# Optimization experiments

Hardware: AMD Instinct MI355X
Metric: run time of the kernel (lower is better)

The kernel has to match this reference:

```python
import jax, jax.numpy as jnp
import numpy as np
from jax.scipy.special import logsumexp

NEG = -1e8
B, M, R, D, H = 32, 24, 384, 2048, 16

def setup_inputs() -> dict:
    key = jax.random.key(0)
    ks = jax.random.split(key, 12)
    inp = {
        'region': jax.random.normal(ks[0], (B, R, D), dtype=jnp.float32),
        'aff': jax.random.normal(ks[1], (B, M, R, 1), dtype=jnp.float32),
        'aff_gt': jax.random.uniform(ks[2], (B, M, R, 1), dtype=jnp.float32),
        'n_mentions': jax.random.randint(ks[3], (B,), 8, M + 1, dtype=jnp.int32),
        'n_regions': jax.random.randint(ks[4], (B,), R // 2, R + 1, dtype=jnp.int32),
        # learned params: tran0/tran1: Linear(d_region,16); tran: Linear(16,1)
        't0_w': jax.random.normal(ks[5], (H, D), dtype=jnp.float32) / np.sqrt(D),
        't0_b': jnp.zeros((H,), dtype=jnp.float32),
        't1_w': jax.random.normal(ks[6], (H, D), dtype=jnp.float32) / np.sqrt(D),
        't1_b': jnp.zeros((H,), dtype=jnp.float32),
        'tr_w': jax.random.normal(ks[7], (1, H), dtype=jnp.float32) / np.sqrt(H),
        'tr_b': jnp.zeros((1,), dtype=jnp.float32),
    }
    return inp


def reference(region, aff, aff_gt, n_mentions, n_regions, t0_w, t0_b, t1_w, t1_b, tr_w, tr_b):
    # masks for padded regions / mentions
    reg_mask = jnp.arange(R)[None, :] < n_regions[:, None]        # (B,R)
    men_mask = jnp.arange(M)[None, :] < n_mentions[:, None]       # (B,M)

    # soft-label normalization (_aff_acti / _aff_norm / _aff_norm_log in torch)
    a = jnp.where(aff_gt[..., 0] >= 0.5, aff_gt[..., 0], 0.0)     # (B,M,R)
    a = a * reg_mask[:, None, :] * men_mask[:, :, None]
    s = a.sum(-1, keepdims=True)
    reward = a / jnp.where(s > 0, s, 1.0)                          # (B,M,R)
    reward_log = jnp.where(reward > 0, jnp.log(jnp.where(reward > 0, reward, 1.0)), NEG)
    active = (s[..., 0] > 0) & men_mask                            # (B,M) mentions with >=1 gold region

    # transition matrix (tran_context='none'): tran[b,i,j] = tran(relu(tran0(r_i)+tran1(r_j)))
    h0 = region @ t0_w.T + t0_b                                    # (B,R,H)
    h1 = region @ t1_w.T + t1_b                                    # (B,R,H)
    h = jax.nn.relu(h0[:, :, None, :] + h1[:, None, :, :])         # (B,R,R,H)
    tran = jnp.einsum('brsh,h->brs', h, tr_w[0]) + tr_b[0]         # (B,R,R): [i=to, j=from]

    emit = aff[..., 0]                                             # (B,M,R)
    alpha0 = jnp.where(reg_mask, 0.0, NEG)                         # padded tags excluded from logsumexp
    score0 = jnp.zeros((B, R), dtype=region.dtype)
    rprev0 = jnp.zeros((B, R), dtype=region.dtype)
    hasp0 = jnp.zeros((B,), dtype=bool)

    def step(carry, xs):
        alpha, score, rprev, hasp = carry
        e, rw, rl, act = xs                                        # (B,R)x3, (B,)
        alpha_t = logsumexp(alpha[:, None, :] + tran, axis=2)      # (B,R)
        score_t = jnp.sum((score[:, None, :] + tran) * rprev[:, None, :], axis=2)
        do_t = (act & hasp)[:, None]
        alpha = jnp.where(do_t, alpha_t, alpha)
        score = jnp.where(do_t, score_t, score)
        am = act[:, None]
        alpha = jnp.where(am, alpha + e, alpha)
        score = jnp.where(am, score + e - rl, score)
        rprev = jnp.where(am, rw, rprev)
        hasp = hasp | act
        return (alpha, score, rprev, hasp), None

    xs = (jnp.moveaxis(emit, 1, 0), jnp.moveaxis(reward, 1, 0),
          jnp.moveaxis(reward_log, 1, 0), active.T)
    (alpha, score, rprev, hasp), _ = jax.lax.scan(step, (alpha0, score0, rprev0, hasp0), xs)

    fwd = logsumexp(alpha, axis=1)                                 # (B,)
    gold = jnp.sum(score * rprev, axis=1)                          # (B,)
    fwd = jnp.where(hasp, fwd, 0.0)
    gold = jnp.where(hasp, gold, 0.0)
    denom = jnp.maximum(n_mentions.sum(), 1).astype(region.dtype)
    return jnp.sum(fwd - gold) / denom
```

## Files before the change

kernel.cpp:

```cpp
#include <hip/hip_runtime.h>

#define NEGV (-100000000.0f)
typedef __attribute__((ext_vector_type(2))) float f32x2;
typedef __attribute__((ext_vector_type(8))) short bf16x8;
typedef __attribute__((ext_vector_type(4))) float f32x4v;

constexpr int BB = 32, MM = 24, RR = 384, DD = 2048;
constexpr int EPITCH = 400;

static __device__ __forceinline__ unsigned pk2bf(float a, float b) {
  unsigned au = __float_as_uint(a) + 0x8000u;
  unsigned bu = __float_as_uint(b) + 0x8000u;
  return (au >> 16) | (bu & 0xffff0000u);
}

__global__ __launch_bounds__(256) void kA(const float* __restrict__ region,
    const float* __restrict__ t0w, const float* __restrict__ t0b,
    const float* __restrict__ t1w, const float* __restrict__ t1b,
    float* __restrict__ h0h1) {
  __shared__ unsigned short Abuf[2][32 * 128];
  __shared__ unsigned short Bbuf[2][32 * 128];
  const int tid = threadIdx.x;
  const int row0 = blockIdx.x * 32;

  const int srow = tid >> 3;
  const int sq = tid & 7;
  const float* aSrc = region + (size_t)(row0 + srow) * DD + sq * 16;
  const float* bSrc = ((srow < 16) ? (t0w + (size_t)srow * DD)
                                   : (t1w + (size_t)(srow - 16) * DD)) + sq * 16;

  auto LOADS = [&](float4* s, int t) {
    const int d0 = t * 128;
#pragma unroll
    for (int i = 0; i < 4; ++i) s[i] = *(const float4*)(aSrc + d0 + i * 4);
#pragma unroll
    for (int i = 0; i < 4; ++i) s[4 + i] = *(const float4*)(bSrc + d0 + i * 4);
  };
  const int wbase = srow * 256 + sq * 32;
  const int wxor = (srow & 7) << 4;
  auto WRITES = [&](const float4* s, int buf) {
    unsigned char* Ab = (unsigned char*)&Abuf[buf][0];
    unsigned char* Bb = (unsigned char*)&Bbuf[buf][0];
#pragma unroll
    for (int i = 0; i < 2; ++i) {
      float4 x = s[i * 2], y = s[i * 2 + 1];
      uint4 pk;
      pk.x = pk2bf(x.x, x.y); pk.y = pk2bf(x.z, x.w);
      pk.z = pk2bf(y.x, y.y); pk.w = pk2bf(y.z, y.w);
      *(uint4*)(Ab + ((wbase + i * 16) ^ wxor)) = pk;
      float4 u = s[4 + i * 2], v = s[4 + i * 2 + 1];
      uint4 qk;
      qk.x = pk2bf(u.x, u.y); qk.y = pk2bf(u.z, u.w);
      qk.z = pk2bf(v.x, v.y); qk.w = pk2bf(v.z, v.w);
      *(uint4*)(Bb + ((wbase + i * 16) ^ wxor)) = qk;
    }
  };

  const int w = tid >> 6;
  const int rt = w & 1;
  const int ht = w >> 1;
  const int lane = tid & 63;
  const int arow = rt * 16 + (lane & 15);
  const int bh = lane & 15;
  const int brow = ht * 16 + bh;
  const int koff = (lane >> 4) * 8;
  const int axor = (arow & 7) << 4;
  const int bxor = (brow & 7) << 4;

  f32x4v acc = {0.f, 0.f, 0.f, 0.f};
  auto MFMAT = [&](int buf) {
    const unsigned char* Ab = (const unsigned char*)&Abuf[buf][0];
    const unsigned char* Bb = (const unsigned char*)&Bbuf[buf][0];
#pragma unroll
    for (int kk = 0; kk < 4; ++kk) {
      const int kb = (kk * 32 + koff) * 2;
      bf16x8 av = *(const bf16x8*)(Ab + ((arow * 256 + kb) ^ axor));
      bf16x8 bv = *(const bf16x8*)(Bb + ((brow * 256 + kb) ^ bxor));
      acc = __builtin_amdgcn_mfma_f32_16x16x32_bf16(av, bv, acc, 0, 0, 0);
    }
  };

  float4 sA[8], sB[8], sC[8];
  LOADS(sA, 0);
  WRITES(sA, 0);
  LOADS(sB, 1);
  LOADS(sC, 2);
  for (int t = 0; t < 16; t += 3) {
    __syncthreads();
    if (t + 1 < 16) WRITES(sB, (t + 1) & 1);
    if (t + 3 < 16) LOADS(sA, t + 3);
    MFMAT(t & 1);
    if (t + 1 < 16) {
      __syncthreads();
      if (t + 2 < 16) WRITES(sC, (t + 2) & 1);
      if (t + 4 < 16) LOADS(sB, t + 4);
      MFMAT((t + 1) & 1);
    }
    if (t + 2 < 16) {
      __syncthreads();
      if (t + 3 < 16) WRITES(sA, (t + 3) & 1);
      if (t + 5 < 16) LOADS(sC, t + 5);
      MFMAT(t & 1);
    }
  }

  const float bias = (ht == 0) ? t0b[bh] : t1b[bh];
#pragma unroll
  for (int i = 0; i < 4; ++i) {
    const int rg = row0 + rt * 16 + (lane >> 4) * 4 + i;
    h0h1[(size_t)rg * 32 + ht * 16 + bh] = acc[i] + bias;
  }
}

__global__ __launch_bounds__(384) void kYT(const float* __restrict__ h0h1,
    const float* __restrict__ trw, const float* __restrict__ trb,
    const float* __restrict__ gt, const float* __restrict__ aff,
    const int* __restrict__ nmen, const int* __restrict__ nreg,
    int* __restrict__ mlist, int* __restrict__ kcnt, float* __restrict__ Em,
    float* __restrict__ bilinP, unsigned char* __restrict__ expb,
    float* __restrict__ expTmax) {
  __shared__ float h1T[16][388];
  __shared__ float h0L[48][16];
  __shared__ float Tl[48][388];
  __shared__ float RP[MM][392];
  __shared__ float part[48][26];
  __shared__ float rsumL[MM], EmL[MM];
  __shared__ int mlistL[MM];
  __shared__ int kcntL;
  const int b = blockIdx.x & 31;
  const int chunk = blockIdx.x >> 5;
  const int r0 = chunk * 48;
  const int tid = threadIdx.x;
  const int lane = tid & 63;
  const int wv = tid >> 6;
  const int nm = nmen[b], nr = nreg[b];

  for (int m = wv; m < MM; m += 6) {
    const size_t bm = (size_t)(b * MM + m);
    float p = 0.f, t1 = 0.f, t2 = 0.f;
#pragma unroll
    for (int i = 0; i < 6; ++i) {
      int s = lane * 6 + i;
      float g = gt[bm * RR + s];
      float a = (g >= 0.5f && s < nr && m < nm) ? g : 0.f;
      float e = aff[bm * RR + s];
      p += a;
      t1 += a * e;
      t2 += (a > 0.f) ? a * __logf(a) : 0.f;
    }
#pragma unroll
    for (int off = 32; off > 0; off >>= 1) {
      p += __shfl_xor(p, off);
      t1 += __shfl_xor(t1, off);
      t2 += __shfl_xor(t2, off);
    }
    if (lane == 0) {
      rsumL[m] = p;
      EmL[m] = (p > 0.f) ? (t1 - t2) / p + __logf(p) : 0.f;
    }
  }
  __syncthreads();
  if (tid == 0) {
    int c = 0;
    for (int m = 0; m < MM; ++m)
      if (rsumL[m] > 0.f) mlistL[c++] = m;
    kcntL = c;
    for (int j = c; j < MM; ++j) mlistL[j] = 0;
  }
  __syncthreads();
  if (chunk == 0 && tid < MM) {
    Em[b * MM + tid] = EmL[tid];
    mlist[b * MM + tid] = mlistL[tid];
    if (tid == 0) kcnt[b] = kcntL;
  }
  const int K = kcntL;

  for (int h = 0; h < 16; ++h)
    for (int s = tid; s < RR; s += 384)
      h1T[h][s] = h0h1[((size_t)b * RR + s) * 32 + 16 + h];
  for (int i = tid; i < 768; i += 384) {
    int row = i >> 4, h = i & 15;
    h0L[row][h] = h0h1[((size_t)b * RR + r0 + row) * 32 + h];
  }
  for (int j = 0; j < MM; ++j) {
    if (j < K) {
      int m = mlistL[j];
      float inv = 1.f / rsumL[m];
      for (int s = tid; s < RR; s += 384) {
        float g = gt[((size_t)(b * MM + m)) * RR + s];
        RP[j][s] = (g >= 0.5f && s < nr) ? g * inv : 0.f;
      }
    } else {
      for (int s = tid; s < RR; s += 384) RP[j][s] = 0.f;
    }
  }
  float w0[16];
#pragma unroll
  for (int h = 0; h < 16; ++h) w0[h] = trw[h];
  const float tb = trb[0];
  __syncthreads();

  const int r = tid >> 3;
  const int jq = tid & 7;
  const int gr = r0 + r;

  for (int i = 0; i < 48; ++i) {
    const int s = jq + 8 * i;
    float a = tb;
#pragma unroll
    for (int h = 0; h < 16; ++h)
      a += fmaxf(h0L[r][h] + h1T[h][s], 0.f) * w0[h];
    Tl[r][s] = a;
  }
  __syncthreads();

  {
    float rmax = -3.0e38f;
    for (int c = 0; c < 48; c += 4) {
      float4 v = *(const float4*)&Tl[r][jq * 48 + c];
      rmax = fmaxf(rmax, fmaxf(fmaxf(v.x, v.y), fmaxf(v.z, v.w)));
    }
    rmax = fmaxf(rmax, __shfl_xor(rmax, 1));
    rmax = fmaxf(rmax, __shfl_xor(rmax, 2));
    rmax = fmaxf(rmax, __shfl_xor(rmax, 4));
    if (jq == 0) expTmax[b * RR + gr] = __expf(rmax);
    unsigned char* obase = expb + ((size_t)b * RR + gr) * RR + jq * 48;
#pragma unroll
    for (int c16 = 0; c16 < 3; ++c16) {
      int w4[4];
#pragma unroll
      for (int ii = 0; ii < 4; ++ii) {
        float4 v = *(const float4*)&Tl[r][jq * 48 + c16 * 16 + ii * 4];
        int pk = __builtin_amdgcn_cvt_pk_fp8_f32(__expf(v.x - rmax),
                                                 __expf(v.y - rmax), 0, false);
        pk = __builtin_amdgcn_cvt_pk_fp8_f32(__expf(v.z - rmax),
                                             __expf(v.w - rmax), pk, true);
        w4[ii] = pk;
      }
      *(int4*)(obase + c16 * 16) = make_int4(w4[0], w4[1], w4[2], w4[3]);
    }
  }

  float acc[3] = {0, 0, 0};
  for (int s0 = 0; s0 < RR; s0 += 4) {
    float4 tv = *(const float4*)&Tl[r][s0];
#pragma unroll
    for (int jj = 0; jj < 3; ++jj) {
      const float4 p0 = *(const float4*)&RP[jq * 3 + jj][s0];
      acc[jj] = fmaf(tv.x, p0.x, acc[jj]);
      acc[jj] = fmaf(tv.y, p0.y, acc[jj]);
      acc[jj] = fmaf(tv.z, p0.z, acc[jj]);
      acc[jj] = fmaf(tv.w, p0.w, acc[jj]);
    }
  }
#pragma unroll
  for (int jj = 0; jj < 3; ++jj) {
    const int jp = jq * 3 + jj;
    const int j = jp + 1;
    part[r][j] = (j < K) ? RP[j][gr] * acc[jj] : 0.f;
  }
  __syncthreads();
  if (tid < MM) {
    const int j = tid;
    float s = 0.f;
    if (j >= 1) {
#pragma unroll 4
      for (int rr2 = 0; rr2 < 48; ++rr2) s += part[rr2][j];
    }
    bilinP[(size_t)(b * 8 + chunk) * MM + j] = s;
  }
}

__global__ __launch_bounds__(512, 1) void kD(
    const unsigned char* __restrict__ expb, const float* __restrict__ expTmax,
    const float* __restrict__ aff, const int* __restrict__ nreg,
    const int* __restrict__ mlist, const int* __restrict__ kcnt,
    const float* __restrict__ Em, const float* __restrict__ bilinP,
    float* __restrict__ result) {
  __shared__ unsigned char eT[RR * EPITCH];
  __shared__ float tf[2][RR];
  __shared__ unsigned int tq[RR / 4];
  __shared__ float wred[2][8];
  __shared__ float fred[8];

  const int b = blockIdx.x;
  const int tid = threadIdx.x;
  const int w = tid >> 6;
  const int lane = tid & 63;
  const int r = lane & 15;
  const int q = lane >> 4;
  const bool act = (r == 0);
  const int nr = nreg[b];

  const int K = kcnt[b];
  if (K == 0) {
    if (tid == 0) result[b] = 0.f;
    return;
  }

  {
    const uint4* src = (const uint4*)(expb + (size_t)b * RR * RR);
#pragma unroll
    for (int j = 0; j < 18; ++j) {
      const int i = tid + j * 512;
      uint4 v = src[i];
      const int row = i / 24;
      const int c = (i - row * 24) * 16;
      *(uint4*)(eT + row * EPITCH + c) = v;
    }
  }
  __syncthreads();

  long long af0[12], af1[12], af2[12];
  {
    const int base = (w * 48 + r) * EPITCH + q * 8;
#pragma unroll
    for (int kt = 0; kt < 12; ++kt) {
      af0[kt] = *(const long long*)(eT + base + kt * 32);
      af1[kt] = *(const long long*)(eT + base + 16 * EPITCH + kt * 32);
      af2[kt] = *(const long long*)(eT + base + 32 * EPITCH + kt * 32);
    }
  }

  float sF4[3][4], eraw4[3][4];
  if (act) {
#pragma unroll
    for (int rt = 0; rt < 3; ++rt) {
      const int rowb = w * 48 + rt * 16 + q * 4;
      *(float4*)sF4[rt] = *(const float4*)&expTmax[b * RR + rowb];
      const int m0 = mlist[b * MM];
      *(float4*)eraw4[rt] =
          *(const float4*)(aff + ((size_t)(b * MM + m0)) * RR + rowb);
    }
  }

  float L = 0.f;

  for (int k = 0; k < K; ++k) {
    const int wpar = (k + 1) & 1;

    float nraw4[3][4] = {{0, 0, 0, 0}, {0, 0, 0, 0}, {0, 0, 0, 0}};
    if (act && k + 1 < K) {
      const int mn = mlist[b * MM + k + 1];
#pragma unroll
      for (int rt = 0; rt < 3; ++rt) {
        const int rowb = w * 48 + rt * 16 + q * 4;
        *(float4*)nraw4[rt] =
            *(const float4*)(aff + ((size_t)(b * MM + mn)) * RR + rowb);
      }
    }

    float tv[3][4] = {{0, 0, 0, 0}, {0, 0, 0, 0}, {0, 0, 0, 0}};
    if (k == 0) {
      if (act) {
#pragma unroll
        for (int rt = 0; rt < 3; ++rt)
#pragma unroll
          for (int i = 0; i < 4; ++i) {
            const int row = w * 48 + rt * 16 + q * 4 + i;
            tv[rt][i] = (row < nr) ? __expf(eraw4[rt][i]) : 0.f;
          }
      }
    } else {
      f32x4v acc0 = {0.f, 0.f, 0.f, 0.f}, acc1 = {0.f, 0.f, 0.f, 0.f},
             acc2 = {0.f, 0.f, 0.f, 0.f};
#pragma unroll
      for (int kt = 0; kt < 12; ++kt) {
        long long bf =
            *(const long long*)((const unsigned char*)tq + kt * 32 + q * 8);
        bf = act ? bf : 0ll;
        acc0 = __builtin_amdgcn_mfma_f32_16x16x32_fp8_fp8(af0[kt], bf, acc0, 0, 0, 0);
        acc1 = __builtin_amdgcn_mfma_f32_16x16x32_fp8_fp8(af1[kt], bf, acc1, 0, 0, 0);
        acc2 = __builtin_amdgcn_mfma_f32_16x16x32_fp8_fp8(af2[kt], bf, acc2, 0, 0, 0);
      }
      if (act) {
#pragma unroll
        for (int i = 0; i < 4; ++i) {
          tv[0][i] = acc0[i] * (__expf(eraw4[0][i]) * sF4[0][i] * 0.00390625f);
          tv[1][i] = acc1[i] * (__expf(eraw4[1][i]) * sF4[1][i] * 0.00390625f);
          tv[2][i] = acc2[i] * (__expf(eraw4[2][i]) * sF4[2][i] * 0.00390625f);
        }
      }
    }

    float lm = 0.f;
    if (act) {
#pragma unroll
      for (int rt = 0; rt < 3; ++rt) {
        const int rowb = w * 48 + rt * 16 + q * 4;
        *(float4*)&tf[wpar][rowb] =
            make_float4(tv[rt][0], tv[rt][1], tv[rt][2], tv[rt][3]);
        lm = fmaxf(lm, fmaxf(fmaxf(tv[rt][0], tv[rt][1]),
                             fmaxf(tv[rt][2], tv[rt][3])));
      }
#pragma unroll
      for (int rt = 0; rt < 3; ++rt)
#pragma unroll
        for (int i = 0; i < 4; ++i) eraw4[rt][i] = nraw4[rt][i];
    }
    lm = fmaxf(lm, __shfl_xor(lm, 16));
    lm = fmaxf(lm, __shfl_xor(lm, 32));
    if (lane == 0) wred[wpar][w] = lm;
    __syncthreads();

    if (k + 1 < K) {
      float4 z0 = *(const float4*)&wred[wpar][0];
      float4 z1 = *(const float4*)&wred[wpar][4];
      float zm = fmaxf(fmaxf(fmaxf(z0.x, z0.y), fmaxf(z0.z, z0.w)),
                       fmaxf(fmaxf(z1.x, z1.y), fmaxf(z1.z, z1.w)));
      L += __logf(zm);
      const float bscale = 256.f / zm;
      if (tid < 96) {
        float4 v = *(const float4*)&tf[wpar][tid * 4];
        int pk = __builtin_amdgcn_cvt_pk_fp8_f32(v.x * bscale, v.y * bscale,
                                                 0, false);
        pk = __builtin_amdgcn_cvt_pk_fp8_f32(v.z * bscale, v.w * bscale,
                                             pk, true);
        tq[tid] = (unsigned)pk;
      }
      __syncthreads();
    }
  }

  const int fpar = K & 1;
  float fp = (tid < RR) ? tf[fpar][tid] : 0.f;
#pragma unroll
  for (int off = 32; off > 0; off >>= 1) fp += __shfl_xor(fp, off);
  if (lane == 0) fred[w] = fp;
  __syncthreads();
  if (tid == 0) {
    float fs = 0.f;
#pragma unroll
    for (int i = 0; i < 8; ++i) fs += fred[i];
    const float fwd = L + __logf(fmaxf(fs, 1e-37f));
    float gold = Em[b * MM + mlist[b * MM + 0]];
    for (int j = 1; j < K; ++j) {
      float bil = 0.f;
#pragma unroll
      for (int c = 0; c < 8; ++c) bil += bilinP[(size_t)(b * 8 + c) * MM + j];
      gold += bil + Em[b * MM + mlist[b * MM + j]];
    }
    result[b] = fwd - gold;
  }
}

__global__ void kE(const float* __restrict__ result, const int* __restrict__ nmen,
                   float* __restrict__ out) {
  if (threadIdx.x == 0 && blockIdx.x == 0) {
    float s = 0.f;
    int d = 0;
    for (int b = 0; b < 32; ++b) { s += result[b]; d += nmen[b]; }
    if (d < 1) d = 1;
    out[0] = s / (float)d;
  }
}

extern "C" void kernel_launch(void* const* d_in, const int* in_sizes, int n_in,
                              void* d_out, int out_size, void* d_ws, size_t ws_size,
                              hipStream_t stream) {
  const float* region = (const float*)d_in[0];
  const float* aff    = (const float*)d_in[1];
  const float* gt     = (const float*)d_in[2];
  const int*   nmen   = (const int*)d_in[3];
  const int*   nreg   = (const int*)d_in[4];
  const float* t0w    = (const float*)d_in[5];
  const float* t0b    = (const float*)d_in[6];
  const float* t1w    = (const float*)d_in[7];
  const float* t1b    = (const float*)d_in[8];
  const float* trw    = (const float*)d_in[9];
  const float* trb    = (const float*)d_in[10];
  float* out = (float*)d_out;
  char* ws = (char*)d_ws;

  size_t off = 0;
  auto alloc = [&](size_t bytes) {
    void* p = ws + off;
    off += (bytes + 255) & ~(size_t)255;
    return p;
  };
  float*         h0h1    = (float*)alloc((size_t)BB * RR * 32 * 4);
  unsigned char* expb    = (unsigned char*)alloc((size_t)BB * RR * RR);
  float*         expTmax = (float*)alloc((size_t)BB * RR * 4);
  int*           mlist   = (int*)alloc((size_t)BB * MM * 4);
  int*           kcnt    = (int*)alloc((size_t)BB * 4);
  float*         Em      = (float*)alloc((size_t)BB * MM * 4);
  float*         bilinP  = (float*)alloc((size_t)BB * 8 * MM * 4);
  float*         result  = (float*)alloc((size_t)BB * 4);

  kA<<<(BB * RR) / 32, 256, 0, stream>>>(region, t0w, t0b, t1w, t1b, h0h1);
  kYT<<<256, 384, 0, stream>>>(h0h1, trw, trb, gt, aff, nmen, nreg,
                               mlist, kcnt, Em, bilinP, expb, expTmax);
  kD<<<BB, 512, 0, stream>>>(expb, expTmax, aff, nreg, mlist, kcnt, Em,
                             bilinP, result);
  kE<<<1, 64, 0, stream>>>(result, nmen, out);
}
```

Measured before the change: 105.5 us.

## Compute transition tile from register-held h1 and use bf16 MFMA for bilinear products

In kYT, each thread now holds its column's h1 vector in registers and reads h0 rows straight from global memory when computing the transition tile. This removes the h1T/h0L shared staging and one barrier. The Tl×RP bilinear reduction moves from scalar FMA loops to bf16 16x16x32 MFMA, with RP padded to 32 rows. Converting to bf16 lowers the precision of the gold-score term, and padding RP adds zero-fill work.

```diff
diff --git a/kernel.cpp b/kernel.cpp
--- a/kernel.cpp
+++ b/kernel.cpp
@@ -119,10 +119,8 @@
     int* __restrict__ mlist, int* __restrict__ kcnt, float* __restrict__ Em,
     float* __restrict__ bilinP, unsigned char* __restrict__ expb,
     float* __restrict__ expTmax) {
-  __shared__ float h1T[16][388];
-  __shared__ float h0L[48][16];
   __shared__ float Tl[48][388];
-  __shared__ float RP[MM][392];
+  __shared__ float RP[32][392];
   __shared__ float part[48][26];
   __shared__ float rsumL[MM], EmL[MM];
   __shared__ int mlistL[MM];
@@ -175,14 +173,7 @@
   }
   const int K = kcntL;
 
-  for (int h = 0; h < 16; ++h)
-    for (int s = tid; s < RR; s += 384)
-      h1T[h][s] = h0h1[((size_t)b * RR + s) * 32 + 16 + h];
-  for (int i = tid; i < 768; i += 384) {
-    int row = i >> 4, h = i & 15;
-    h0L[row][h] = h0h1[((size_t)b * RR + r0 + row) * 32 + h];
-  }
-  for (int j = 0; j < MM; ++j) {
+  for (int j = 0; j < 32; ++j) {
     if (j < K) {
       int m = mlistL[j];
       float inv = 1.f / rsumL[m];
@@ -194,27 +185,43 @@
       for (int s = tid; s < RR; s += 384) RP[j][s] = 0.f;
     }
   }
+
   float w0[16];
 #pragma unroll
   for (int h = 0; h < 16; ++h) w0[h] = trw[h];
   const float tb = trb[0];
+  const int s = tid;
+  float h1r[16];
+  {
+    const float* hp = h0h1 + ((size_t)b * RR + s) * 32 + 16;
+    *(float4*)&h1r[0] = *(const float4*)(hp);
+    *(float4*)&h1r[4] = *(const float4*)(hp + 4);
+    *(float4*)&h1r[8] = *(const float4*)(hp + 8);
+    *(float4*)&h1r[12] = *(const float4*)(hp + 12);
+  }
+  for (int r4 = 0; r4 < 48; r4 += 4) {
+    const float* p0 = h0h1 + ((size_t)b * RR + r0 + r4) * 32;
+    float a0 = tb, a1 = tb, a2 = tb, a3 = tb;
+#pragma unroll
+    for (int h = 0; h < 16; ++h) {
+      const float hv = h1r[h];
+      const float wvv = w0[h];
+      a0 += fmaxf(p0[h] + hv, 0.f) * wvv;
+      a1 += fmaxf(p0[32 + h] + hv, 0.f) * wvv;
+      a2 += fmaxf(p0[64 + h] + hv, 0.f) * wvv;
+      a3 += fmaxf(p0[96 + h] + hv, 0.f) * wvv;
+    }
+    Tl[r4][s] = a0;
+    Tl[r4 + 1][s] = a1;
+    Tl[r4 + 2][s] = a2;
+    Tl[r4 + 3][s] = a3;
+  }
   __syncthreads();
 
-  const int r = tid >> 3;
-  const int jq = tid & 7;
-  const int gr = r0 + r;
-
-  for (int i = 0; i < 48; ++i) {
-    const int s = jq + 8 * i;
-    float a = tb;
-#pragma unroll
-    for (int h = 0; h < 16; ++h)
-      a += fmaxf(h0L[r][h] + h1T[h][s], 0.f) * w0[h];
-    Tl[r][s] = a;
-  }
-  __syncthreads();
-
   {
+    const int r = tid >> 3;
+    const int jq = tid & 7;
+    const int gr = r0 + r;
     float rmax = -3.0e38f;
     for (int c = 0; c < 48; c += 4) {
       float4 v = *(const float4*)&Tl[r][jq * 48 + c];
@@ -241,33 +248,44 @@
     }
   }
 
-  float acc[3] = {0, 0, 0};
-  for (int s0 = 0; s0 < RR; s0 += 4) {
-    float4 tv = *(const float4*)&Tl[r][s0];
-#pragma unroll
-    for (int jj = 0; jj < 3; ++jj) {
-      const float4 p0 = *(const float4*)&RP[jq * 3 + jj][s0];
-      acc[jj] = fmaf(tv.x, p0.x, acc[jj]);
-      acc[jj] = fmaf(tv.y, p0.y, acc[jj]);
-      acc[jj] = fmaf(tv.z, p0.z, acc[jj]);
-      acc[jj] = fmaf(tv.w, p0.w, acc[jj]);
-    }
-  }
-#pragma unroll
-  for (int jj = 0; jj < 3; ++jj) {
-    const int jp = jq * 3 + jj;
-    const int j = jp + 1;
-    part[r][j] = (j < K) ? RP[j][gr] * acc[jj] : 0.f;
+  {
+    const int mtile = wv >> 1;
+    const int ntile = wv & 1;
+    const int lrow = mtile * 16 + (lane & 15);
+    const int jcol = ntile * 16 + (lane & 15);
+    const int koff = (lane >> 4) * 8;
+    f32x4v accY = {0.f, 0.f, 0.f, 0.f};
+#pragma unroll
+    for (int kt = 0; kt < 12; ++kt) {
+      const int kb = kt * 32 + koff;
+      float4 av0 = *(const float4*)&Tl[lrow][kb];
+      float4 av1 = *(const float4*)&Tl[lrow][kb + 4];
+      float4 bv0 = *(const float4*)&RP[jcol][kb];
+      float4 bv1 = *(const float4*)&RP[jcol][kb + 4];
+      union { unsigned u[4]; bf16x8 v; } Af, Bf;
+      Af.u[0] = pk2bf(av0.x, av0.y); Af.u[1] = pk2bf(av0.z, av0.w);
+      Af.u[2] = pk2bf(av1.x, av1.y); Af.u[3] = pk2bf(av1.z, av1.w);
+      Bf.u[0] = pk2bf(bv0.x, bv0.y); Bf.u[1] = pk2bf(bv0.z, bv0.w);
+      Bf.u[2] = pk2bf(bv1.x, bv1.y); Bf.u[3] = pk2bf(bv1.z, bv1.w);
+      accY = __builtin_amdgcn_mfma_f32_16x16x32_bf16(Af.v, Bf.v, accY, 0, 0, 0);
+    }
+#pragma unroll
+    for (int i = 0; i < 4; ++i) {
+      const int orow = mtile * 16 + (lane >> 4) * 4 + i;
+      const int jp = ntile * 16 + (lane & 15);
+      const int j = jp + 1;
+      if (j < 26) part[orow][j] = (j < K) ? RP[j][r0 + orow] * accY[i] : 0.f;
+    }
   }
   __syncthreads();
   if (tid < MM) {
     const int j = tid;
-    float s = 0.f;
+    float sm = 0.f;
     if (j >= 1) {
 #pragma unroll 4
-      for (int rr2 = 0; rr2 < 48; ++rr2) s += part[rr2][j];
-    }
-    bilinP[(size_t)(b * 8 + chunk) * MM + j] = s;
+      for (int rr2 = 0; rr2 < 48; ++rr2) sm += part[rr2][j];
+    }
+    bilinP[(size_t)(b * 8 + chunk) * MM + j] = sm;
   }
 }
 
```

New measurement: 121.3 us. +15.0%, slower.
